# Optimization experiments

Hardware: AMD Instinct MI355X
Metric: run time of the kernel (lower is better)

The kernel has to match this reference:

```python
import jax, jax.numpy as jnp
import numpy as np

LOOKUP_WINDOW = 101  # module init arg
EPS = 1e-12  # F.normalize eps


def setup_inputs() -> dict:
    key = jax.random.key(0)
    k1, k2, k3 = jax.random.split(key, 3)
    B, T, F_IN, D = 4, 2048, 2048, 128
    x = jax.random.normal(k1, (B, T, F_IN), dtype=jnp.float32)
    # nn.Linear(in_filters, output_dim); stored here as [in, out] so y = x @ W + b
    W = jax.random.normal(k2, (F_IN, D), dtype=jnp.float32) / np.sqrt(F_IN).astype(np.float32)
    b = jax.random.normal(k3, (D,), dtype=jnp.float32) * 0.01
    return {"x": x, "W": W, "b": b}


def reference(x, W, b):
    hw = LOOKUP_WINDOW // 2
    # projection + L2 normalize over feature dim (F.normalize p=2, dim=-1)
    p = x @ W + b  # [B,T,D]
    p = p / jnp.maximum(jnp.linalg.norm(p, axis=-1, keepdims=True), EPS)
    B, T, D = p.shape
    # zero-pad along time so out-of-range neighbors contribute 0 similarity
    pp = jnp.pad(p, ((0, 0), (hw, hw), (0, 0)))  # [B, T+2*hw, D]
    # window gather: idx[t, w] = t + w indexes padded time axis (neighbor t + w - hw)
    idx = jnp.arange(T)[:, None] + jnp.arange(LOOKUP_WINDOW)[None, :]  # [T, W]
    windows = pp[:, idx, :]  # [B, T, W, D]
    # banded similarity: sim[b,t,w] = <p[b,t], neighbor at offset w-hw>
    sim = jnp.einsum('btd,btwd->btw', p, windows)
    return sim  # [B, T, LOOKUP_WINDOW]
```

## Files before the change

kernel.cpp:

```cpp
#include <hip/hip_runtime.h>
#include <hip/hip_bf16.h>

#define T_LEN 2048
#define D_DIM 128
#define K_DIM 2048
#define M_DIM 8192
#define LOOKUP 101
#define HWIN 50

typedef __attribute__((ext_vector_type(8))) short short8;
typedef __attribute__((ext_vector_type(4))) float f32x4;

static __device__ __forceinline__ unsigned int f2bf(float f) {
  unsigned int u = __float_as_uint(f);
  return (u + 0x7fffu + ((u >> 16) & 1u)) >> 16;
}
static __device__ __forceinline__ float bflo(unsigned int u) { return __uint_as_float(u << 16); }
static __device__ __forceinline__ float bfhi(unsigned int u) { return __uint_as_float(u & 0xffff0000u); }

static __device__ __forceinline__ short8 pack8(float4 lo, float4 hi) {
  uint4 u;
  u.x = f2bf(lo.x) | (f2bf(lo.y) << 16);
  u.y = f2bf(lo.z) | (f2bf(lo.w) << 16);
  u.z = f2bf(hi.x) | (f2bf(hi.y) << 16);
  u.w = f2bf(hi.z) | (f2bf(hi.w) << 16);
  return *(short8*)&u;
}

typedef __attribute__((address_space(3))) unsigned char lds_uchar;
typedef const __attribute__((address_space(1))) unsigned char g_uchar;
static __device__ __forceinline__ void gll16(const void* g, void* l) {
  __builtin_amdgcn_global_load_lds((g_uchar*)g, (lds_uchar*)l, 16, 0, 0);
}

__global__ __launch_bounds__(256) void k_pack(const float* __restrict__ W,
                                              unsigned short* __restrict__ Bp) {
  __shared__ float sw[32][132];
  const int ks = blockIdx.x;
  const int t = threadIdx.x;
  const float* src = W + (size_t)ks * 32 * D_DIM;
#pragma unroll
  for (int j = 0; j < 4; ++j) {
    int idx = t + j * 256;
    int row = idx >> 5, c4 = idx & 31;
    float4 v = *(const float4*)(src + row * D_DIM + c4 * 4);
    *(float4*)&sw[row][c4 * 4] = v;
  }
  __syncthreads();
#pragma unroll
  for (int e = 0; e < 2; ++e) {
    int f = t * 2 + e;
    int ct = f >> 6, l = f & 63;
    int kr = (l >> 4) * 8, col = ct * 16 + (l & 15);
    uint4 o;
    o.x = f2bf(sw[kr + 0][col]) | (f2bf(sw[kr + 1][col]) << 16);
    o.y = f2bf(sw[kr + 2][col]) | (f2bf(sw[kr + 3][col]) << 16);
    o.z = f2bf(sw[kr + 4][col]) | (f2bf(sw[kr + 5][col]) << 16);
    o.w = f2bf(sw[kr + 6][col]) | (f2bf(sw[kr + 7][col]) << 16);
    *(uint4*)(Bp + (((size_t)(ks * 8 + ct) << 6) + l) * 8) = o;
  }
}

__global__ __launch_bounds__(512, 4) void k_gemm(const float* __restrict__ X,
                                                 const unsigned short* __restrict__ Bp,
                                                 const float* __restrict__ bias,
                                                 unsigned short* __restrict__ Pn) {
  __shared__ __align__(16) unsigned char smem[65536];
  const int tid = threadIdx.x;
  const int lane = tid & 63;
  const int wv = tid >> 6;
  const int r0 = blockIdx.x * 16;
  const int l15 = lane & 15;
  const int kg = lane >> 4;

  unsigned char* Ab = smem + wv * 8192;
  const int srow = lane >> 5;
  const int scol = lane & 31;

  f32x4 acc[8];
#pragma unroll
  for (int i = 0; i < 8; ++i) acc[i] = (f32x4){0.f, 0.f, 0.f, 0.f};

  for (int c = 0; c < 2; ++c) {
#pragma unroll
    for (int i = 0; i < 8; ++i) {
      int r = 2 * i + srow;
      int gsrc = scol ^ (r & 7);
      const float* src = X + (size_t)(r0 + r) * K_DIM + wv * 256 + c * 128 + gsrc * 4;
      gll16(src, Ab + i * 1024);
    }
    asm volatile("s_waitcnt vmcnt(0)" ::: "memory");
    __builtin_amdgcn_sched_barrier(0);
#pragma unroll
    for (int s = 0; s < 4; ++s) {
      int g0 = s * 8 + kg * 2;
      float4 alo = *(const float4*)(Ab + l15 * 512 + (((g0 + 0) ^ (l15 & 7)) << 4));
      float4 ahi = *(const float4*)(Ab + l15 * 512 + (((g0 + 1) ^ (l15 & 7)) << 4));
      short8 af = pack8(alo, ahi);
      int ksg = wv * 8 + c * 4 + s;
#pragma unroll
      for (int ct = 0; ct < 8; ++ct) {
        short8 bf = *(const short8*)(Bp + (((size_t)(ksg * 8 + ct) << 6) + lane) * 8);
        acc[ct] = __builtin_amdgcn_mfma_f32_16x16x32_bf16(af, bf, acc[ct], 0, 0, 0);
      }
    }
  }

  float* Pw = (float*)Ab;
#pragma unroll
  for (int ct = 0; ct < 8; ++ct)
#pragma unroll
    for (int j = 0; j < 4; ++j)
      Pw[(kg * 4 + j) * 128 + ct * 16 + l15] = acc[ct][j];
  __syncthreads();

  const int row = tid >> 5;
  const int c4 = tid & 31;
  float4 tot = make_float4(0.f, 0.f, 0.f, 0.f);
#pragma unroll
  for (int q = 0; q < 8; ++q) {
    float4 v = *(const float4*)(smem + q * 8192 + row * 512 + c4 * 16);
    tot.x += v.x; tot.y += v.y; tot.z += v.z; tot.w += v.w;
  }
  float4 bv = *(const float4*)(bias + c4 * 4);
  tot.x += bv.x; tot.y += bv.y; tot.z += bv.z; tot.w += bv.w;
  float ss = tot.x * tot.x + tot.y * tot.y + tot.z * tot.z + tot.w * tot.w;
  ss += __shfl_xor(ss, 1);
  ss += __shfl_xor(ss, 2);
  ss += __shfl_xor(ss, 4);
  ss += __shfl_xor(ss, 8);
  ss += __shfl_xor(ss, 16);
  float sc = 1.0f / fmaxf(sqrtf(ss), 1e-12f);
  unsigned int p0 = f2bf(tot.x * sc) | (f2bf(tot.y * sc) << 16);
  unsigned int p1 = f2bf(tot.z * sc) | (f2bf(tot.w * sc) << 16);
  *(uint2*)(Pn + (size_t)(r0 + row) * D_DIM + c4 * 4) = make_uint2(p0, p1);
}

#define SROWS 144

__global__ __launch_bounds__(256) void k_sim(const unsigned short* __restrict__ Pn,
                                             float* __restrict__ out) {
  __shared__ unsigned short sm[SROWS * D_DIM];
  const int bb = blockIdx.x >> 6;
  const int tb = blockIdx.x & 63;
  const int t0 = tb * 32;
  const int tid = threadIdx.x;

  for (int idx = tid; idx < SROWS * 16; idx += 256) {
    int i = idx >> 4, seg = idx & 15;
    int t = t0 - HWIN + i;
    uint4 val = make_uint4(0u, 0u, 0u, 0u);
    if (t >= 0 && t < T_LEN)
      val = *(const uint4*)(Pn + ((size_t)bb * T_LEN + t) * D_DIM + seg * 8);
    *(uint4*)&sm[i * D_DIM + ((seg ^ (i & 7)) << 3)] = val;
  }
  __syncthreads();

  const int lane = tid & 63;
  const int wv = tid >> 6;
  const int l15 = lane & 15;
  const int kg = lane >> 4;
  const int rt = wv >> 1;
  const int itp = wv & 1;

  short8 af[4];
  const int ia = HWIN + rt * 16 + l15;
#pragma unroll
  for (int ks = 0; ks < 4; ++ks) {
    int g = ks * 4 + kg;
    af[ks] = *(const short8*)&sm[ia * D_DIM + ((g ^ (ia & 7)) << 3)];
  }

  for (int it = itp; it < 9; it += 2) {
    f32x4 acc = (f32x4){0.f, 0.f, 0.f, 0.f};
    const int ib = it * 16 + l15;
#pragma unroll
    for (int ks = 0; ks < 4; ++ks) {
      int g = ks * 4 + kg;
      short8 bf = *(const short8*)&sm[ib * D_DIM + ((g ^ (ib & 7)) << 3)];
      acc = __builtin_amdgcn_mfma_f32_16x16x32_bf16(af[ks], bf, acc, 0, 0, 0);
    }
#pragma unroll
    for (int j = 0; j < 4; ++j) {
      int r = rt * 16 + kg * 4 + j;
      int w = ib - r;
      if (w >= 0 && w <= 100)
        out[((size_t)bb * T_LEN + t0 + r) * LOOKUP + w] = acc[j];
    }
  }
}

extern "C" void kernel_launch(void* const* d_in, const int* in_sizes, int n_in,
                              void* d_out, int out_size, void* d_ws, size_t ws_size,
                              hipStream_t stream) {
  (void)in_sizes; (void)n_in; (void)out_size; (void)ws_size;
  const float* x = (const float*)d_in[0];
  const float* W = (const float*)d_in[1];
  const float* b = (const float*)d_in[2];
  float* out = (float*)d_out;
  unsigned short* Bp = (unsigned short*)d_ws;
  unsigned short* Pn = Bp + (size_t)D_DIM * K_DIM;

  k_pack<<<64, 256, 0, stream>>>(W, Bp);
  k_gemm<<<M_DIM / 16, 512, 0, stream>>>(x, Bp, b, Pn);
  k_sim<<<4 * (T_LEN / 32), 256, 0, stream>>>(Pn, out);
}
```

Baseline: 34.33 us.

## Restructure projection GEMM with double-buffered LDS staging and per-wave column split

The GEMM block now covers 32 rows instead of 16 and double-buffers X tiles in 136KB of LDS, prefetching the next stage with global_load_lds while computing the current one. Each wave owns one 16-column slice of the output across the full K range, which removes the cross-wave reduction over eight partial sums. W fragments are ping-ponged in registers, and blocks alternate which K half they start with to spread memory traffic. The large LDS footprint cuts occupancy to one block per CU, and only 256 blocks are launched.

New measurement: 66.87 us. +94.8%, slower.

```diff
diff --git a/kernel.cpp b/kernel.cpp
--- a/kernel.cpp
+++ b/kernel.cpp
@@ -15,16 +15,14 @@
   unsigned int u = __float_as_uint(f);
   return (u + 0x7fffu + ((u >> 16) & 1u)) >> 16;
 }
-static __device__ __forceinline__ float bflo(unsigned int u) { return __uint_as_float(u << 16); }
-static __device__ __forceinline__ float bfhi(unsigned int u) { return __uint_as_float(u & 0xffff0000u); }
-
-static __device__ __forceinline__ short8 pack8(float4 lo, float4 hi) {
-  uint4 u;
-  u.x = f2bf(lo.x) | (f2bf(lo.y) << 16);
-  u.y = f2bf(lo.z) | (f2bf(lo.w) << 16);
-  u.z = f2bf(hi.x) | (f2bf(hi.y) << 16);
-  u.w = f2bf(hi.z) | (f2bf(hi.w) << 16);
-  return *(short8*)&u;
+
+static __device__ __forceinline__ short8 pack8v(float4 lo, float4 hi) {
+  union { short8 s; __hip_bfloat162 h[4]; } u;
+  u.h[0] = __float22bfloat162_rn(make_float2(lo.x, lo.y));
+  u.h[1] = __float22bfloat162_rn(make_float2(lo.z, lo.w));
+  u.h[2] = __float22bfloat162_rn(make_float2(hi.x, hi.y));
+  u.h[3] = __float22bfloat162_rn(make_float2(hi.z, hi.w));
+  return u.s;
 }
 
 typedef __attribute__((address_space(3))) unsigned char lds_uchar;
@@ -61,79 +59,117 @@
   }
 }
 
-__global__ __launch_bounds__(512, 4) void k_gemm(const float* __restrict__ X,
-                                                 const unsigned short* __restrict__ Bp,
-                                                 const float* __restrict__ bias,
-                                                 unsigned short* __restrict__ Pn) {
-  __shared__ __align__(16) unsigned char smem[65536];
+__global__ __launch_bounds__(512) void k_gemm(const float* __restrict__ X,
+                                              const unsigned short* __restrict__ Bp,
+                                              const float* __restrict__ bias,
+                                              unsigned short* __restrict__ Pn) {
+  __shared__ __align__(16) unsigned char xb[2][65536];
+  __shared__ __align__(16) unsigned char Pq[8192];
   const int tid = threadIdx.x;
   const int lane = tid & 63;
   const int wv = tid >> 6;
-  const int r0 = blockIdx.x * 16;
+  const int r0 = blockIdx.x * 32;
   const int l15 = lane & 15;
   const int kg = lane >> 4;
-
-  unsigned char* Ab = smem + wv * 8192;
-  const int srow = lane >> 5;
-  const int scol = lane & 31;
-
-  f32x4 acc[8];
-#pragma unroll
-  for (int i = 0; i < 8; ++i) acc[i] = (f32x4){0.f, 0.f, 0.f, 0.f};
-
-  for (int c = 0; c < 2; ++c) {
+  const int hA = blockIdx.x & 1;
+  const int hB = hA ^ 1;
+
+  auto stage = [&](int sl, int rgb, int h) {
 #pragma unroll
     for (int i = 0; i < 8; ++i) {
-      int r = 2 * i + srow;
-      int gsrc = scol ^ (r & 7);
-      const float* src = X + (size_t)(r0 + r) * K_DIM + wv * 256 + c * 128 + gsrc * 4;
-      gll16(src, Ab + i * 1024);
-    }
-    asm volatile("s_waitcnt vmcnt(0)" ::: "memory");
-    __builtin_amdgcn_sched_barrier(0);
-#pragma unroll
-    for (int s = 0; s < 4; ++s) {
-      int g0 = s * 8 + kg * 2;
-      float4 alo = *(const float4*)(Ab + l15 * 512 + (((g0 + 0) ^ (l15 & 7)) << 4));
-      float4 ahi = *(const float4*)(Ab + l15 * 512 + (((g0 + 1) ^ (l15 & 7)) << 4));
-      short8 af = pack8(alo, ahi);
-      int ksg = wv * 8 + c * 4 + s;
-#pragma unroll
-      for (int ct = 0; ct < 8; ++ct) {
-        short8 bf = *(const short8*)(Bp + (((size_t)(ksg * 8 + ct) << 6) + lane) * 8);
-        acc[ct] = __builtin_amdgcn_mfma_f32_16x16x32_bf16(af, bf, acc[ct], 0, 0, 0);
-      }
-    }
-  }
-
-  float* Pw = (float*)Ab;
-#pragma unroll
-  for (int ct = 0; ct < 8; ++ct)
-#pragma unroll
-    for (int j = 0; j < 4; ++j)
-      Pw[(kg * 4 + j) * 128 + ct * 16 + l15] = acc[ct][j];
-  __syncthreads();
-
-  const int row = tid >> 5;
-  const int c4 = tid & 31;
-  float4 tot = make_float4(0.f, 0.f, 0.f, 0.f);
-#pragma unroll
-  for (int q = 0; q < 8; ++q) {
-    float4 v = *(const float4*)(smem + q * 8192 + row * 512 + c4 * 16);
-    tot.x += v.x; tot.y += v.y; tot.z += v.z; tot.w += v.w;
-  }
-  float4 bv = *(const float4*)(bias + c4 * 4);
-  tot.x += bv.x; tot.y += bv.y; tot.z += bv.z; tot.w += bv.w;
-  float ss = tot.x * tot.x + tot.y * tot.y + tot.z * tot.z + tot.w * tot.w;
-  ss += __shfl_xor(ss, 1);
-  ss += __shfl_xor(ss, 2);
-  ss += __shfl_xor(ss, 4);
-  ss += __shfl_xor(ss, 8);
-  ss += __shfl_xor(ss, 16);
-  float sc = 1.0f / fmaxf(sqrtf(ss), 1e-12f);
-  unsigned int p0 = f2bf(tot.x * sc) | (f2bf(tot.y * sc) << 16);
-  unsigned int p1 = f2bf(tot.z * sc) | (f2bf(tot.w * sc) << 16);
-  *(uint2*)(Pn + (size_t)(r0 + row) * D_DIM + c4 * 4) = make_uint2(p0, p1);
+      int id = wv * 8 + i;
+      int row = id >> 2, kb = id & 3;
+      const float* src = X + (size_t)(r0 + rgb + row) * K_DIM + h * 1024 + kb * 256 +
+                         ((lane ^ (row & 7)) << 2);
+      gll16(src, xb[sl] + row * 4096 + kb * 1024 + lane * 16);
+    }
+  };
+#define LOADB(P, KB)                                                                  \
+  {                                                                                   \
+    _Pragma("unroll") for (int s = 0; s < 4; ++s)                                     \
+        P[s] = *(const short8*)(Bp + (((size_t)((KB) + s) * 8 + wv) * 64 + lane) * 8); \
+  }
+
+  short8 ba[4], bb[4];
+  f32x4 acc = (f32x4){0.f, 0.f, 0.f, 0.f};
+  const float4 bvp = *(const float4*)(bias + (tid & 31) * 4);
+
+  stage(0, 0, hA);
+  LOADB(ba, hA * 32);
+  asm volatile("s_waitcnt vmcnt(4)" ::: "memory");
+  __builtin_amdgcn_s_barrier();
+  __builtin_amdgcn_sched_barrier(0);
+
+#pragma unroll
+  for (int p = 0; p < 4; ++p) {
+    const int sl = p & 1;
+    if (p < 3) {
+      const int pn = p + 1;
+      stage(pn & 1, (pn >> 1) * 16, (pn & 1) ? hB : hA);
+    }
+#pragma unroll
+    for (int c = 0; c < 8; ++c) {
+      const int t = p * 8 + c;
+      if (t < 31) {
+        const int pn = (t + 1) >> 3, cn = (t + 1) & 7;
+        const int hn = (pn & 1) ? hB : hA;
+        if ((t & 1) == 0) LOADB(bb, hn * 32 + cn * 4)
+        else              LOADB(ba, hn * 32 + cn * 4)
+      }
+      if (p < 3) {
+        asm volatile("s_waitcnt vmcnt(12)" ::: "memory");
+      } else if (c < 7) {
+        asm volatile("s_waitcnt vmcnt(4)" ::: "memory");
+      } else {
+        asm volatile("s_waitcnt vmcnt(0)" ::: "memory");
+      }
+      const unsigned char* xgp = xb[sl] + l15 * 4096;
+#pragma unroll
+      for (int s = 0; s < 4; ++s) {
+        int sg = c * 32 + s * 8 + kg * 2;
+        float4 alo = *(const float4*)(xgp + ((sg ^ (l15 & 7)) << 4));
+        float4 ahi = *(const float4*)(xgp + (((sg + 1) ^ (l15 & 7)) << 4));
+        short8 xf = pack8v(alo, ahi);
+        short8 wf = ((t & 1) == 0) ? ba[s] : bb[s];
+        acc = __builtin_amdgcn_mfma_f32_16x16x32_bf16(wf, xf, acc, 0, 0, 0);
+      }
+    }
+    if (p < 3) {
+      asm volatile("s_waitcnt vmcnt(4)" ::: "memory");
+      __builtin_amdgcn_s_barrier();
+      __builtin_amdgcn_sched_barrier(0);
+    }
+    if (p == 1 || p == 3) {
+      const int rgb = (p >> 1) * 16;
+      {
+        int gq = wv * 4 + kg;
+        int wbyte = l15 * 512 + ((gq << 4) ^ ((l15 & 7) << 4));
+        *(float4*)(Pq + wbyte) = make_float4(acc[0], acc[1], acc[2], acc[3]);
+      }
+      asm volatile("s_waitcnt lgkmcnt(0)" ::: "memory");
+      __builtin_amdgcn_s_barrier();
+      __builtin_amdgcn_sched_barrier(0);
+      {
+        int row = tid >> 5;
+        int c4 = tid & 31;
+        float4 v = *(const float4*)(Pq + row * 512 + ((c4 << 4) ^ ((row & 7) << 4)));
+        float t0v = v.x + bvp.x, t1v = v.y + bvp.y, t2v = v.z + bvp.z, t3v = v.w + bvp.w;
+        float ss = t0v * t0v + t1v * t1v + t2v * t2v + t3v * t3v;
+        ss += __shfl_xor(ss, 1);
+        ss += __shfl_xor(ss, 2);
+        ss += __shfl_xor(ss, 4);
+        ss += __shfl_xor(ss, 8);
+        ss += __shfl_xor(ss, 16);
+        float sc = 1.0f / fmaxf(sqrtf(ss), 1e-12f);
+        uint2 o;
+        o.x = f2bf(t0v * sc) | (f2bf(t1v * sc) << 16);
+        o.y = f2bf(t2v * sc) | (f2bf(t3v * sc) << 16);
+        *(uint2*)(Pn + (size_t)(r0 + rgb + row) * D_DIM + c4 * 4) = o;
+      }
+      acc = (f32x4){0.f, 0.f, 0.f, 0.f};
+      __builtin_amdgcn_s_barrier();
+    }
+  }
 }
 
 #define SROWS 144
@@ -202,6 +238,6 @@
   unsigned short* Pn = Bp + (size_t)D_DIM * K_DIM;
 
   k_pack<<<64, 256, 0, stream>>>(W, Bp);
-  k_gemm<<<M_DIM / 16, 512, 0, stream>>>(x, Bp, b, Pn);
+  k_gemm<<<M_DIM / 32, 512, 0, stream>>>(x, Bp, b, Pn);
   k_sim<<<4 * (T_LEN / 32), 256, 0, stream>>>(Pn, out);
 }
```
